# Kernel optimization log

Measured on AMD Instinct MI355X. Metric: run time of the kernel, lower is better.

Reference implementation:

```python
import jax, jax.numpy as jnp
import numpy as np

G = 512      # graphs per batch
PER = 800    # nodes per graph
N = G * PER  # total nodes
X = 256      # x_size (= h_size so layers compose)
H = 256      # h_size
VOCAB = 32000
NCLS = 104


def setup_inputs() -> dict:
    rng = np.random.default_rng(0)
    # Random tree per graph: node 0 is root, parent(i) uniform in [0, i)
    i_idx = np.arange(1, PER)
    parents = np.floor(rng.random((G, PER - 1)) * i_idx).astype(np.int64)
    base = (np.arange(G) * PER)[:, None]
    edge_dst = (parents + base).reshape(-1)                     # parent (message receiver)
    edge_src = (np.tile(np.arange(1, PER), (G, 1)) + base).reshape(-1)  # child
    E = edge_src.size
    child_count = np.bincount(edge_dst, minlength=N)
    # sort edges by (dst, src) so child position = rank among siblings
    order = np.lexsort((edge_src, edge_dst))
    edge_src = edge_src[order]
    edge_dst = edge_dst[order]
    starts = np.cumsum(child_count) - child_count
    pos = np.arange(E) - starts[edge_dst]
    n = child_count[edge_dst]
    # position-dependent interpolation coefficient: n==1 -> (W_l+W_r)/2 i.e. alpha=0.5
    alpha = np.where(n == 1, 0.5, pos / np.maximum(n - 1, 1)).astype(np.float32)

    node_type = rng.integers(0, VOCAB, N).astype(np.int32)
    graph_ids = np.repeat(np.arange(G), PER).astype(np.int32)

    key = jax.random.key(0)
    ks = jax.random.split(key, 6)
    s = 0.05
    emb = jax.random.normal(ks[0], (VOCAB, X), jnp.float32) * s
    W_left = jax.random.normal(ks[1], (X, H), jnp.float32) * s
    W_right = jax.random.normal(ks[2], (X, H), jnp.float32) * s
    W_top = jax.random.normal(ks[3], (X, H), jnp.float32) * s
    b_conv = jnp.zeros((H,), jnp.float32)
    gate_w = jax.random.normal(ks[4], (H, 1), jnp.float32) * s
    gate_b = jnp.zeros((1,), jnp.float32)
    cls_w = jax.random.normal(ks[5], (H, NCLS), jnp.float32) * s
    cls_b = jnp.zeros((NCLS,), jnp.float32)

    return dict(
        node_type=jnp.asarray(node_type), edge_src=jnp.asarray(edge_src.astype(np.int32)),
        edge_dst=jnp.asarray(edge_dst.astype(np.int32)), alpha=jnp.asarray(alpha),
        child_count=jnp.asarray(child_count.astype(np.int32)), graph_ids=jnp.asarray(graph_ids),
        emb=emb, W_left=W_left, W_right=W_right, W_top=W_top, b_conv=b_conv,
        gate_w=gate_w, gate_b=gate_b, cls_w=cls_w, cls_b=cls_b,
    )


def reference(node_type, edge_src, edge_dst, alpha, child_count, graph_ids,
              emb, W_left, W_right, W_top, b_conv,
              gate_w, gate_b, cls_w, cls_b):
    h = emb[node_type]                                  # [N, X]
    # TBCNN conv layer: sum_i ((1-a_i) W_left + a_i W_right) h_child_i
    #                 = (sum (1-a_i) h_i) W_left + (sum a_i h_i) W_right
    h_src = h[edge_src]                                 # [E, X]
    left = jax.ops.segment_sum(h_src * (1.0 - alpha)[:, None], edge_dst, num_segments=N)
    right = jax.ops.segment_sum(h_src * alpha[:, None], edge_dst, num_segments=N)
    conv = jax.nn.relu(left @ W_left + right @ W_right + h @ W_top + b_conv)
    # nodes without children receive no message -> keep embedding (DGL semantics)
    h = jnp.where((child_count > 0)[:, None], conv, h)  # [N, H]

    # GlobalAttentionPooling: per-graph softmax over gate scores
    gate = h @ gate_w + gate_b                          # [N, 1]
    gmax = jax.ops.segment_max(gate, graph_ids, num_segments=G)
    e = jnp.exp(gate - gmax[graph_ids])
    denom = jax.ops.segment_sum(e, graph_ids, num_segments=G)
    attn = e / denom[graph_ids]                         # [N, 1]
    pooled = jax.ops.segment_sum(h * attn, graph_ids, num_segments=G)  # [G, H]

    return pooled @ cls_w + cls_b                       # [G, NCLS]
```

## Files before the change

kernel.cpp:

```cpp
#include <hip/hip_runtime.h>
#include <stdint.h>

#define XH   256
#define NCLS 104

typedef _Float16 half2v __attribute__((ext_vector_type(2)));
typedef _Float16 half4v __attribute__((ext_vector_type(4)));
typedef _Float16 half8v __attribute__((ext_vector_type(8)));
typedef __attribute__((ext_vector_type(4))) float floatx4;

__device__ __forceinline__ void gll16(const void* g, void* l) {
    __builtin_amdgcn_global_load_lds(
        (const __attribute__((address_space(1))) unsigned*)g,
        (__attribute__((address_space(3))) unsigned*)l, 16, 0, 0);
}
__device__ __forceinline__ float fdot2f(half2v a, half2v b, float c) {
#if __has_builtin(__builtin_amdgcn_fdot2)
    return __builtin_amdgcn_fdot2(a, b, c, false);
#else
    return c + (float)a[0] * (float)b[0] + (float)a[1] * (float)b[1];
#endif
}
__device__ __forceinline__ int MF(int x) { return (x + (x >> 2)) & 3; }


__global__ __launch_bounds__(256)
void k_prep(const float* __restrict__ Wl, const float* __restrict__ Wr,
            const float* __restrict__ Wt,
            const int* __restrict__ edge_src, const int* __restrict__ edge_dst,
            const float* __restrict__ alpha, const int* __restrict__ node_type,
            _Float16* __restrict__ Btw, int2* __restrict__ epk,
            int* __restrict__ row_start, int VQ, int E) {
    int idx = blockIdx.x * 256 + threadIdx.x;
    if (idx < 3 * XH * XH) {
        int n = idx >> 8, k = idx & 255;
        int m, c;
        if (n < 512) { m = n & 1; c = n >> 1; }
        else         { m = 2;     c = n - 512; }
        const float* W = (m == 0) ? Wl : (m == 1) ? Wr : Wt;
        Btw[idx] = (_Float16)W[k * XH + c];
        return;
    }
    idx -= 3 * XH * XH;
    if (idx < E) {
        int s  = edge_src[idx];
        float a = alpha[idx];
        int ts = node_type[s];
        int x;
        if      (a == 0.0f) x = 2 * VQ + ts * 256;
        else if (a == 1.0f) x = 3 * VQ + ts * 256;
        else if (a == 0.5f) x = 4 * VQ + ts * 256;
        else                x = (ts * 512) | 1;
        half2v w = { (_Float16)(1.f - a), (_Float16)a };
        int2 p;
        p.x = x;
        p.y = __builtin_bit_cast(int, w);
        epk[idx] = p;
        int d = edge_dst[idx];
        if (idx == 0 || edge_dst[idx - 1] != d) row_start[d] = idx;
    }
}

__global__ __launch_bounds__(512)
void k_main(const float* __restrict__ emb, const _Float16* __restrict__ Btw,
            const float* __restrict__ b_conv, _Float16* __restrict__ W16, int VQ) {
    __shared__ __align__(16) _Float16 Ab[8][64][32];
    __shared__ __align__(16) _Float16 Bb[2][128][32];

    const int tid  = threadIdx.x;
    const int lane = tid & 63;
    const int wv   = tid >> 6;
    const int m0   = blockIdx.x * 64;
    const int mw   = wv >> 2;
    const int nw   = wv & 3;
    const int quad = lane >> 4;
    const int l15  = lane & 15;

    {
        const int kh  = tid >> 8;
        const int u   = tid & 255;
        const int row = u >> 2, rem = u & 3;
        const int slot = rem ^ MF(row & 15);
        #pragma unroll
        for (int kc2 = 0; kc2 < 4; kc2++) {
            int kc = kc2 * 2 + kh;
            const float* ga = &emb[(size_t)(m0 + row) * XH + kc * 32 + rem * 8];
            floatx4 f0 = *(const floatx4*)ga;
            floatx4 f1 = *(const floatx4*)(ga + 4);
            half8v h;
            #pragma unroll
            for (int i = 0; i < 4; i++) { h[i] = (_Float16)f0[i]; h[4 + i] = (_Float16)f1[i]; }
            *(half8v*)&Ab[kc][row][slot * 8] = h;
            *(half8v*)&W16[(size_t)6 * VQ + (size_t)(m0 + row) * XH + kc * 32 + rem * 8] = h;
        }
    }
    const int brow = tid >> 2, pslot = tid & 3;
    const int bd = pslot ^ MF(brow & 15);
    gll16((const char*)Btw + (size_t)brow * 512 + bd * 16,
          (char*)&Bb[0][0][0] + wv * 1024);
    __syncthreads();

    int buf = 0;
    for (int ng = 0; ng < 6; ng++) {
        floatx4 acc[2][2];
        #pragma unroll
        for (int i = 0; i < 2; i++)
            #pragma unroll
            for (int j = 0; j < 2; j++) acc[i][j] = floatx4{0.f, 0.f, 0.f, 0.f};

        #pragma unroll
        for (int kc = 0; kc < 8; kc++) {
            int ni = ng * 8 + kc + 1;
            if (ni < 48) {
                int nng = ni >> 3, nkc = ni & 7;
                gll16((const char*)Btw + (size_t)(nng * 128 + brow) * 512 + nkc * 64 + bd * 16,
                      (char*)&Bb[buf ^ 1][0][0] + wv * 1024);
            }
            half8v a[2], b[2];
            #pragma unroll
            for (int mt = 0; mt < 2; mt++)
                a[mt] = *(const half8v*)&Ab[kc][mw * 32 + mt * 16 + l15][(quad ^ MF(l15)) * 8];
            #pragma unroll
            for (int nt = 0; nt < 2; nt++)
                b[nt] = *(const half8v*)&Bb[buf][nw * 32 + nt * 16 + l15][(quad ^ MF(l15)) * 8];
            #pragma unroll
            for (int nt = 0; nt < 2; nt++)
                #pragma unroll
                for (int mt = 0; mt < 2; mt++)
                    acc[mt][nt] = __builtin_amdgcn_mfma_f32_16x16x32_f16(a[mt], b[nt], acc[mt][nt], 0, 0, 0);
            __syncthreads();
            buf ^= 1;
        }

        const bool isT = (ng >= 4);
        #pragma unroll
        for (int nt = 0; nt < 2; nt++) {
            int col = ng * 128 + nw * 32 + nt * 16 + l15;
            float bias = isT ? b_conv[col - 512] : 0.f;
            #pragma unroll
            for (int mt = 0; mt < 2; mt++) {
                #pragma unroll
                for (int r = 0; r < 4; r++) {
                    int row = m0 + mw * 32 + mt * 16 + quad * 4 + r;
                    float v = acc[mt][nt][r] + bias;
                    if (isT) {
                        W16[(size_t)5 * VQ + (size_t)row * 256 + (col - 512)] = (_Float16)v;
                    } else {
                        W16[(size_t)row * 512 + col] = (_Float16)v;
                        float pv = __shfl_xor(v, 1);
                        int cp = col >> 1;
                        if ((col & 1) == 0) {
                            W16[(size_t)2 * VQ + (size_t)row * 256 + cp] = (_Float16)v;
                            W16[(size_t)4 * VQ + (size_t)row * 256 + cp] = (_Float16)(0.5f * (v + pv));
                        } else {
                            W16[(size_t)3 * VQ + (size_t)row * 256 + cp] = (_Float16)v;
                        }
                    }
                }
            }
        }
    }
}

__global__ __launch_bounds__(1024, 8)
void k_graph(const int* __restrict__ nty, const int* __restrict__ cc,
             const _Float16* __restrict__ W16,
             const int2* __restrict__ epk, const int* __restrict__ row_start,
             const float* __restrict__ gate_w, const float* __restrict__ gate_b,
             const float* __restrict__ cls_w, const float* __restrict__ cls_b,
             float* __restrict__ out, int PER, int VQ) {
    const int g    = blockIdx.x;
    const int tid  = threadIdx.x;
    const int lane = tid & 63;
    const int wv   = tid >> 6;
    const int base = g * PER;

    __shared__ float pw[16 * XH];
    __shared__ float ds[16];
    __shared__ float pooled[XH];

    float gw4[4];
    #pragma unroll
    for (int i = 0; i < 4; i++) gw4[i] = gate_w[4 * lane + i];
    const float gb = gate_b[0];

    float acc4[4] = {0.f, 0.f, 0.f, 0.f};
    float dsum = 0.f;

    int vg = base + wv;
    int c  = cc[vg];
    int tv = nty[vg];
    int rs = (c > 0) ? row_start[vg] : 0;
    half4v yt = *(const half4v*)&W16[(size_t)(c == 0 ? 6 : 5) * VQ + (size_t)tv * 256 + 4 * lane];
    int2 pd0 = epk[rs];

    for (int v = wv; v < PER; v += 16) {
        const bool has = (v + 16 < PER);
        const int vns = has ? vg + 16 : vg;
        int cn  = has ? cc[vns] : 0;
        int tvn = nty[vns];
        int rsn = (has && cn > 0) ? row_start[vns] : 0;
        half4v ytn = *(const half4v*)&W16[(size_t)(cn == 0 ? 6 : 5) * VQ + (size_t)tvn * 256 + 4 * lane];
        int2 pdn = epk[rsn];

        float h4[4];
        if (c == 0) {
            #pragma unroll
            for (int i = 0; i < 4; i++) h4[i] = (float)yt[i];
        } else {
            float s4[4] = {0.f, 0.f, 0.f, 0.f};
            int2 p = pd0;
            int e = rs + 1;
            const int e1 = rs + c;
            while (true) {
                if (p.x & 1) {
                    half8v y = *(const half8v*)&W16[(size_t)(p.x ^ 1) + 8 * lane];
                    half2v w = __builtin_bit_cast(half2v, p.y);
                    #pragma unroll
                    for (int i = 0; i < 4; i++)
                        s4[i] = fdot2f(half2v{y[2 * i], y[2 * i + 1]}, w, s4[i]);
                } else {
                    half4v y = *(const half4v*)&W16[(size_t)p.x + 4 * lane];
                    #pragma unroll
                    for (int i = 0; i < 4; i++) s4[i] += (float)y[i];
                }
                if (e >= e1) break;
                p = epk[e++];
            }
            #pragma unroll
            for (int i = 0; i < 4; i++)
                h4[i] = fmaxf(s4[i] + (float)yt[i], 0.f);
        }

        float sg = h4[0] * gw4[0] + h4[1] * gw4[1] + h4[2] * gw4[2] + h4[3] * gw4[3];
        #pragma unroll
        for (int o = 1; o < 64; o <<= 1) sg += __shfl_xor(sg, o);
        float ew = __expf(sg + gb);
        dsum += ew;
        #pragma unroll
        for (int i = 0; i < 4; i++) acc4[i] += ew * h4[i];

        c = cn; rs = rsn; yt = ytn; pd0 = pdn; vg = vns;
    }

    #pragma unroll
    for (int i = 0; i < 4; i++) pw[wv * XH + 4 * lane + i] = acc4[i];
    if (lane == 0) ds[wv] = dsum;
    __syncthreads();

    if (tid < XH) {
        float p = 0.f, d = 0.f;
        #pragma unroll
        for (int w = 0; w < 16; w++) p += pw[w * XH + tid];
        #pragma unroll
        for (int w = 0; w < 16; w++) d += ds[w];
        pooled[tid] = p / d;
    }
    __syncthreads();

    if (tid < NCLS) {
        float o = cls_b[tid];
        #pragma unroll 8
        for (int k = 0; k < XH; k++) o += pooled[k] * cls_w[k * NCLS + tid];
        out[g * NCLS + tid] = o;
    }
}

extern "C" void kernel_launch(void* const* d_in, const int* in_sizes, int n_in,
                              void* d_out, int out_size, void* d_ws, size_t ws_size,
                              hipStream_t stream) {
    const int*   node_type   = (const int*)d_in[0];
    const int*   edge_src    = (const int*)d_in[1];
    const int*   edge_dst    = (const int*)d_in[2];
    const float* alpha       = (const float*)d_in[3];
    const int*   child_count = (const int*)d_in[4];
    const float* emb         = (const float*)d_in[6];
    const float* Wl          = (const float*)d_in[7];
    const float* Wr          = (const float*)d_in[8];
    const float* Wt          = (const float*)d_in[9];
    const float* b_conv      = (const float*)d_in[10];
    const float* gate_w      = (const float*)d_in[11];
    const float* gate_b      = (const float*)d_in[12];
    const float* cls_w       = (const float*)d_in[13];
    const float* cls_b       = (const float*)d_in[14];

    const int N     = in_sizes[0];
    const int E     = in_sizes[1];
    const int vocab = in_sizes[6] / XH;
    const int G     = out_size / NCLS;
    const int PER   = N / G;
    const int VQ    = vocab * 256;

    _Float16* W16 = (_Float16*)d_ws;
    _Float16* Btw = W16 + (size_t)7 * VQ;
    int2*     epk = (int2*)(Btw + 3 * XH * XH);
    int*      row_start = (int*)(epk + E);

    hipLaunchKernelGGL(k_prep, dim3((3 * XH * XH + E + 255) / 256), dim3(256), 0, stream,
                       Wl, Wr, Wt, edge_src, edge_dst, alpha, node_type,
                       Btw, epk, row_start, VQ, E);

    hipLaunchKernelGGL(k_main, dim3(vocab / 64), dim3(512), 0, stream,
                       emb, Btw, b_conv, W16, VQ);

    hipLaunchKernelGGL(k_graph, dim3(G), dim3(1024), 0, stream,
                       node_type, child_count, W16, epk, row_start,
                       gate_w, gate_b, cls_w, cls_b, (float*)d_out, PER, VQ);
}
```

Baseline: 250.0 us.

## Drop interleaved projection table, restage GEMM epilogue via LDS, unroll edge gather

The vocab projection table loses its interleaved left/right copy: general-alpha edges now gather from the separate left and right tables and blend them with fdot2, which shrinks the workspace from seven to five vocab-sized planes. k_main is retiled to 32 rows per block with each wave owning 96 output columns. Its epilogue goes through swizzled LDS so the left, right, mid and top tables are written as coalesced vector stores. The graph kernel's per-node edge loop is unrolled by two with prefetch of the next packed edge. General edges now issue two 8-byte loads instead of one 16-byte load, and k_main needs more LDS per block.

```diff
diff --git a/kernel.cpp b/kernel.cpp
--- a/kernel.cpp
+++ b/kernel.cpp
@@ -47,11 +47,11 @@
         float a = alpha[idx];
         int ts = node_type[s];
         int x;
-        if      (a == 0.0f) x = 2 * VQ + ts * 256;
-        else if (a == 1.0f) x = 3 * VQ + ts * 256;
-        else if (a == 0.5f) x = 4 * VQ + ts * 256;
-        else                x = (ts * 512) | 1;
-        half2v w = { (_Float16)(1.f - a), (_Float16)a };
+        half2v w;
+        if      (a == 0.0f) { x = ts * 256;          w = half2v{1.0f16, 0.0f16}; }
+        else if (a == 1.0f) { x = VQ + ts * 256;     w = half2v{1.0f16, 0.0f16}; }
+        else if (a == 0.5f) { x = 2 * VQ + ts * 256; w = half2v{1.0f16, 0.0f16}; }
+        else { x = (ts * 256) | 1; w = half2v{(_Float16)(1.f - a), (_Float16)a}; }
         int2 p;
         p.x = x;
         p.y = __builtin_bit_cast(int, w);
@@ -61,104 +61,134 @@
     }
 }
 
-__global__ __launch_bounds__(512)
+__global__ __launch_bounds__(512, 4)
 void k_main(const float* __restrict__ emb, const _Float16* __restrict__ Btw,
             const float* __restrict__ b_conv, _Float16* __restrict__ W16, int VQ) {
-    __shared__ __align__(16) _Float16 Ab[8][64][32];
-    __shared__ __align__(16) _Float16 Bb[2][128][32];
+    __shared__ __align__(16) _Float16 Ab[32 * 256];
+    __shared__ __align__(16) _Float16 Bb[768 * 32];
 
     const int tid  = threadIdx.x;
     const int lane = tid & 63;
     const int wv   = tid >> 6;
-    const int m0   = blockIdx.x * 64;
-    const int mw   = wv >> 2;
-    const int nw   = wv & 3;
     const int quad = lane >> 4;
     const int l15  = lane & 15;
+    const int m0   = blockIdx.x * 32;
 
     {
-        const int kh  = tid >> 8;
-        const int u   = tid & 255;
-        const int row = u >> 2, rem = u & 3;
-        const int slot = rem ^ MF(row & 15);
-        #pragma unroll
-        for (int kc2 = 0; kc2 < 4; kc2++) {
-            int kc = kc2 * 2 + kh;
-            const float* ga = &emb[(size_t)(m0 + row) * XH + kc * 32 + rem * 8];
-            floatx4 f0 = *(const floatx4*)ga;
-            floatx4 f1 = *(const floatx4*)(ga + 4);
-            half8v h;
-            #pragma unroll
-            for (int i = 0; i < 4; i++) { h[i] = (_Float16)f0[i]; h[4 + i] = (_Float16)f1[i]; }
-            *(half8v*)&Ab[kc][row][slot * 8] = h;
-            *(half8v*)&W16[(size_t)6 * VQ + (size_t)(m0 + row) * XH + kc * 32 + rem * 8] = h;
-        }
-    }
-    const int brow = tid >> 2, pslot = tid & 3;
-    const int bd = pslot ^ MF(brow & 15);
-    gll16((const char*)Btw + (size_t)brow * 512 + bd * 16,
-          (char*)&Bb[0][0][0] + wv * 1024);
-    __syncthreads();
-
-    int buf = 0;
-    for (int ng = 0; ng < 6; ng++) {
-        floatx4 acc[2][2];
-        #pragma unroll
-        for (int i = 0; i < 2; i++)
-            #pragma unroll
-            for (int j = 0; j < 2; j++) acc[i][j] = floatx4{0.f, 0.f, 0.f, 0.f};
-
-        #pragma unroll
-        for (int kc = 0; kc < 8; kc++) {
-            int ni = ng * 8 + kc + 1;
-            if (ni < 48) {
-                int nng = ni >> 3, nkc = ni & 7;
-                gll16((const char*)Btw + (size_t)(nng * 128 + brow) * 512 + nkc * 64 + bd * 16,
-                      (char*)&Bb[buf ^ 1][0][0] + wv * 1024);
-            }
-            half8v a[2], b[2];
+        int row = tid >> 4;
+        int cg  = tid & 15;
+        const float* ga = &emb[(size_t)(m0 + row) * XH + cg * 16];
+        floatx4 f0 = *(const floatx4*)ga;
+        floatx4 f1 = *(const floatx4*)(ga + 4);
+        floatx4 f2 = *(const floatx4*)(ga + 8);
+        floatx4 f3 = *(const floatx4*)(ga + 12);
+        half8v h0, h1;
+        #pragma unroll
+        for (int i = 0; i < 4; i++) {
+            h0[i] = (_Float16)f0[i]; h0[4 + i] = (_Float16)f1[i];
+            h1[i] = (_Float16)f2[i]; h1[4 + i] = (_Float16)f3[i];
+        }
+        int g0 = cg * 2, g1 = cg * 2 + 1;
+        *(half8v*)&Ab[row * 256 + (g0 >> 2) * 32 + ((g0 & 3) ^ MF(row & 15)) * 8] = h0;
+        *(half8v*)&Ab[row * 256 + (g1 >> 2) * 32 + ((g1 & 3) ^ MF(row & 15)) * 8] = h1;
+        _Float16* ep = &W16[(size_t)4 * VQ + (size_t)(m0 + row) * 256 + cg * 16];
+        *(half8v*)ep = h0;
+        *(half8v*)(ep + 8) = h1;
+    }
+
+    auto stageB = [&](int kc) {
+        #pragma unroll
+        for (int i = 0; i < 6; i++) {
+            int grp = wv * 6 + i;
+            int row = grp * 16 + (lane >> 2);
+            int bd  = (lane & 3) ^ MF(row & 15);
+            gll16((const char*)Btw + (size_t)row * 512 + kc * 64 + bd * 16,
+                  (char*)Bb + grp * 1024);
+        }
+    };
+    stageB(0);
+
+    floatx4 acc[6][2];
+    #pragma unroll
+    for (int i = 0; i < 6; i++)
+        #pragma unroll
+        for (int j = 0; j < 2; j++) acc[i][j] = floatx4{0.f, 0.f, 0.f, 0.f};
+
+    const int nbase = wv * 96;
+    for (int kc = 0; kc < 8; kc++) {
+        __syncthreads();
+        half8v af[6], bf[2];
+        #pragma unroll
+        for (int nt = 0; nt < 6; nt++) {
+            int row = nbase + nt * 16 + l15;
+            af[nt] = *(const half8v*)&Bb[row * 32 + ((quad ^ MF(l15)) * 8)];
+        }
+        #pragma unroll
+        for (int mt = 0; mt < 2; mt++) {
+            int row = mt * 16 + l15;
+            bf[mt] = *(const half8v*)&Ab[row * 256 + kc * 32 + ((quad ^ MF(l15)) * 8)];
+        }
+        __syncthreads();
+        if (kc < 7) stageB(kc + 1);
+        #pragma unroll
+        for (int nt = 0; nt < 6; nt++)
             #pragma unroll
             for (int mt = 0; mt < 2; mt++)
-                a[mt] = *(const half8v*)&Ab[kc][mw * 32 + mt * 16 + l15][(quad ^ MF(l15)) * 8];
+                acc[nt][mt] = __builtin_amdgcn_mfma_f32_16x16x32_f16(af[nt], bf[mt], acc[nt][mt], 0, 0, 0);
+    }
+
+    #pragma unroll
+    for (int nt = 0; nt < 6; nt++) {
+        #pragma unroll
+        for (int mt = 0; mt < 2; mt++) {
+            int m  = mt * 16 + l15;
+            int n0 = nbase + nt * 16 + quad * 4;
+            half4v hv;
             #pragma unroll
-            for (int nt = 0; nt < 2; nt++)
-                b[nt] = *(const half8v*)&Bb[buf][nw * 32 + nt * 16 + l15][(quad ^ MF(l15)) * 8];
-            #pragma unroll
-            for (int nt = 0; nt < 2; nt++)
-                #pragma unroll
-                for (int mt = 0; mt < 2; mt++)
-                    acc[mt][nt] = __builtin_amdgcn_mfma_f32_16x16x32_f16(a[mt], b[nt], acc[mt][nt], 0, 0, 0);
-            __syncthreads();
-            buf ^= 1;
-        }
-
-        const bool isT = (ng >= 4);
-        #pragma unroll
-        for (int nt = 0; nt < 2; nt++) {
-            int col = ng * 128 + nw * 32 + nt * 16 + l15;
-            float bias = isT ? b_conv[col - 512] : 0.f;
-            #pragma unroll
-            for (int mt = 0; mt < 2; mt++) {
-                #pragma unroll
-                for (int r = 0; r < 4; r++) {
-                    int row = m0 + mw * 32 + mt * 16 + quad * 4 + r;
-                    float v = acc[mt][nt][r] + bias;
-                    if (isT) {
-                        W16[(size_t)5 * VQ + (size_t)row * 256 + (col - 512)] = (_Float16)v;
-                    } else {
-                        W16[(size_t)row * 512 + col] = (_Float16)v;
-                        float pv = __shfl_xor(v, 1);
-                        int cp = col >> 1;
-                        if ((col & 1) == 0) {
-                            W16[(size_t)2 * VQ + (size_t)row * 256 + cp] = (_Float16)v;
-                            W16[(size_t)4 * VQ + (size_t)row * 256 + cp] = (_Float16)(0.5f * (v + pv));
-                        } else {
-                            W16[(size_t)3 * VQ + (size_t)row * 256 + cp] = (_Float16)v;
-                        }
-                    }
-                }
-            }
-        }
+            for (int r = 0; r < 4; r++) hv[r] = (_Float16)acc[nt][mt][r];
+            int gs = (n0 >> 2) ^ (m & 7);
+            *(half4v*)((char*)Bb + (size_t)m * 1536 + gs * 8) = hv;
+        }
+    }
+    __syncthreads();
+
+    #pragma unroll
+    for (int it = 0; it < 4; it++) {
+        int u = it * 512 + tid;
+        int m = u >> 6, ns = u & 63;
+        int q0 = ((ns * 8) >> 2) ^ (m & 7);
+        int q1 = (((ns * 8) >> 2) + 1) ^ (m & 7);
+        half4v v0 = *(const half4v*)((const char*)Bb + (size_t)m * 1536 + q0 * 8);
+        half4v v1 = *(const half4v*)((const char*)Bb + (size_t)m * 1536 + q1 * 8);
+        float l0 = (float)v0[0], r0 = (float)v0[1], l1 = (float)v0[2], r1 = (float)v0[3];
+        float l2 = (float)v1[0], r2 = (float)v1[1], l3 = (float)v1[2], r3 = (float)v1[3];
+        half4v yl = { (_Float16)l0, (_Float16)l1, (_Float16)l2, (_Float16)l3 };
+        half4v yr = { (_Float16)r0, (_Float16)r1, (_Float16)r2, (_Float16)r3 };
+        half4v ym = { (_Float16)(0.5f * (l0 + r0)), (_Float16)(0.5f * (l1 + r1)),
+                      (_Float16)(0.5f * (l2 + r2)), (_Float16)(0.5f * (l3 + r3)) };
+        size_t ro = (size_t)(m0 + m) * 256 + ns * 4;
+        *(half4v*)&W16[ro]          = yl;
+        *(half4v*)&W16[VQ + ro]     = yr;
+        *(half4v*)&W16[2 * VQ + ro] = ym;
+    }
+    #pragma unroll
+    for (int it = 0; it < 2; it++) {
+        int u = it * 512 + tid;
+        int m = u >> 5, ns = u & 31;
+        int n0 = 512 + ns * 8;
+        int q0 = (n0 >> 2) ^ (m & 7);
+        int q1 = ((n0 >> 2) + 1) ^ (m & 7);
+        half4v v0 = *(const half4v*)((const char*)Bb + (size_t)m * 1536 + q0 * 8);
+        half4v v1 = *(const half4v*)((const char*)Bb + (size_t)m * 1536 + q1 * 8);
+        floatx4 b0 = *(const floatx4*)&b_conv[ns * 8];
+        floatx4 b1 = *(const floatx4*)&b_conv[ns * 8 + 4];
+        half8v o;
+        #pragma unroll
+        for (int i = 0; i < 4; i++) {
+            o[i]     = (_Float16)((float)v0[i] + b0[i]);
+            o[4 + i] = (_Float16)((float)v1[i] + b1[i]);
+        }
+        *(half8v*)&W16[(size_t)3 * VQ + (size_t)(m0 + m) * 256 + ns * 8] = o;
     }
 }
 
@@ -168,7 +198,7 @@
              const int2* __restrict__ epk, const int* __restrict__ row_start,
              const float* __restrict__ gate_w, const float* __restrict__ gate_b,
              const float* __restrict__ cls_w, const float* __restrict__ cls_b,
-             float* __restrict__ out, int PER, int VQ) {
+             float* __restrict__ out, int PER, int VQ, int E) {
     const int g    = blockIdx.x;
     const int tid  = threadIdx.x;
     const int lane = tid & 63;
@@ -191,7 +221,7 @@
     int c  = cc[vg];
     int tv = nty[vg];
     int rs = (c > 0) ? row_start[vg] : 0;
-    half4v yt = *(const half4v*)&W16[(size_t)(c == 0 ? 6 : 5) * VQ + (size_t)tv * 256 + 4 * lane];
+    half4v yt = *(const half4v*)&W16[(size_t)(c == 0 ? 4 : 3) * VQ + (size_t)tv * 256 + 4 * lane];
     int2 pd0 = epk[rs];
 
     for (int v = wv; v < PER; v += 16) {
@@ -200,7 +230,7 @@
         int cn  = has ? cc[vns] : 0;
         int tvn = nty[vns];
         int rsn = (has && cn > 0) ? row_start[vns] : 0;
-        half4v ytn = *(const half4v*)&W16[(size_t)(cn == 0 ? 6 : 5) * VQ + (size_t)tvn * 256 + 4 * lane];
+        half4v ytn = *(const half4v*)&W16[(size_t)(cn == 0 ? 4 : 3) * VQ + (size_t)tvn * 256 + 4 * lane];
         int2 pdn = epk[rsn];
 
         float h4[4];
@@ -209,23 +239,37 @@
             for (int i = 0; i < 4; i++) h4[i] = (float)yt[i];
         } else {
             float s4[4] = {0.f, 0.f, 0.f, 0.f};
-            int2 p = pd0;
-            int e = rs + 1;
+            int e = rs;
             const int e1 = rs + c;
-            while (true) {
-                if (p.x & 1) {
-                    half8v y = *(const half8v*)&W16[(size_t)(p.x ^ 1) + 8 * lane];
-                    half2v w = __builtin_bit_cast(half2v, p.y);
-                    #pragma unroll
-                    for (int i = 0; i < 4; i++)
-                        s4[i] = fdot2f(half2v{y[2 * i], y[2 * i + 1]}, w, s4[i]);
-                } else {
-                    half4v y = *(const half4v*)&W16[(size_t)p.x + 4 * lane];
-                    #pragma unroll
-                    for (int i = 0; i < 4; i++) s4[i] += (float)y[i];
-                }
-                if (e >= e1) break;
-                p = epk[e++];
+            int2 p0 = pd0;
+            while (e + 2 <= e1) {
+                int2 p1 = epk[e + 1];
+                int2 pn = epk[min(e + 2, E - 1)];
+                int off0 = p0.x & ~1, d0 = (p0.x & 1) ? VQ : 0;
+                int off1 = p1.x & ~1, d1 = (p1.x & 1) ? VQ : 0;
+                half4v a0 = *(const half4v*)&W16[(size_t)off0 + 4 * lane];
+                half4v b0 = *(const half4v*)&W16[(size_t)(off0 + d0) + 4 * lane];
+                half4v a1 = *(const half4v*)&W16[(size_t)off1 + 4 * lane];
+                half4v b1 = *(const half4v*)&W16[(size_t)(off1 + d1) + 4 * lane];
+                half2v w0 = __builtin_bit_cast(half2v, p0.y);
+                half2v w1 = __builtin_bit_cast(half2v, p1.y);
+                #pragma unroll
+                for (int i = 0; i < 4; i++)
+                    s4[i] = fdot2f(half2v{a0[i], b0[i]}, w0, s4[i]);
+                #pragma unroll
+                for (int i = 0; i < 4; i++)
+                    s4[i] = fdot2f(half2v{a1[i], b1[i]}, w1, s4[i]);
+                p0 = pn;
+                e += 2;
+            }
+            if (e < e1) {
+                int off0 = p0.x & ~1, d0 = (p0.x & 1) ? VQ : 0;
+                half4v a0 = *(const half4v*)&W16[(size_t)off0 + 4 * lane];
+                half4v b0 = *(const half4v*)&W16[(size_t)(off0 + d0) + 4 * lane];
+                half2v w0 = __builtin_bit_cast(half2v, p0.y);
+                #pragma unroll
+                for (int i = 0; i < 4; i++)
+                    s4[i] = fdot2f(half2v{a0[i], b0[i]}, w0, s4[i]);
             }
             #pragma unroll
             for (int i = 0; i < 4; i++)
@@ -292,7 +336,7 @@
     const int VQ    = vocab * 256;
 
     _Float16* W16 = (_Float16*)d_ws;
-    _Float16* Btw = W16 + (size_t)7 * VQ;
+    _Float16* Btw = W16 + (size_t)5 * VQ;
     int2*     epk = (int2*)(Btw + 3 * XH * XH);
     int*      row_start = (int*)(epk + E);
 
@@ -300,10 +344,10 @@
                        Wl, Wr, Wt, edge_src, edge_dst, alpha, node_type,
                        Btw, epk, row_start, VQ, E);
 
-    hipLaunchKernelGGL(k_main, dim3(vocab / 64), dim3(512), 0, stream,
+    hipLaunchKernelGGL(k_main, dim3(vocab / 32), dim3(512), 0, stream,
                        emb, Btw, b_conv, W16, VQ);
 
     hipLaunchKernelGGL(k_graph, dim3(G), dim3(1024), 0, stream,
                        node_type, child_count, W16, epk, row_start,
-                       gate_w, gate_b, cls_w, cls_b, (float*)d_out, PER, VQ);
-}
+                       gate_w, gate_b, cls_w, cls_b, (float*)d_out, PER, VQ, E);
+}
```

After: 234.8 us. -6.1%, faster.
